# Optimization experiments

Measured on AMD Instinct MI355X. Metric: run time of the kernel, lower is better.

Reference implementation:

```python
import jax, jax.numpy as jnp
import numpy as np

D = 768       # GATv2 in/out feats (num_heads=1)
D_OUT = 384   # fc output
K = 51        # round(top_rate * L) = round(0.1 * 512)
EPS = 1e-5    # nn.LayerNorm default eps


def _layer_norm(x, g, b):
    mu = jnp.mean(x, axis=-1, keepdims=True)
    var = jnp.mean((x - mu) ** 2, axis=-1, keepdims=True)
    return (x - mu) / jnp.sqrt(var + EPS) * g + b


def setup_inputs() -> dict:
    key = jax.random.key(0)
    ks = jax.random.split(key, 12)
    B, L = 4, 512
    s = 0.02
    return {
        "hidden_state": jax.random.normal(ks[0], (B, L, D), jnp.float32),
        "attention": jax.random.uniform(ks[1], (B, L, L), jnp.float32),
        # GATv2Conv params (fc_src, fc_dst, attn vector, output bias)
        "W_src": jax.random.normal(ks[2], (D, D), jnp.float32) * s,
        "b_src": jnp.zeros((D,), jnp.float32),
        "W_dst": jax.random.normal(ks[3], (D, D), jnp.float32) * s,
        "b_dst": jnp.zeros((D,), jnp.float32),
        "attn_vec": jax.random.normal(ks[4], (D,), jnp.float32) * s,
        "gat_bias": jnp.zeros((D,), jnp.float32),
        # GlobalAttentionPooling gate_nn: Linear(768, 1)
        "gate_W": jax.random.normal(ks[5], (D, 1), jnp.float32) * s,
        "gate_b": jnp.zeros((1,), jnp.float32),
        # LayerNorm(768)
        "ln_g": jnp.ones((D,), jnp.float32),
        "ln_b": jnp.zeros((D,), jnp.float32),
        # fc: Linear(768, 384)
        "fc_W": jax.random.normal(ks[6], (D, D_OUT), jnp.float32) * s,
        "fc_b": jnp.zeros((D_OUT,), jnp.float32),
        # LayerNorm(384)
        "ln2_g": jnp.ones((D_OUT,), jnp.float32),
        "ln2_b": jnp.zeros((D_OUT,), jnp.float32),
        "mask": jnp.ones((B, L), jnp.int32),  # unused by the original forward
        "type": 0,                              # unused string/type flag
    }


def reference(hidden_state, attention, W_src, b_src, W_dst, b_dst, attn_vec,
              gat_bias, gate_W, gate_b, ln_g, ln_b, fc_W, fc_b, ln2_g, ln2_b,
              mask, type):
    B, L, _ = hidden_state.shape
    # --- topk sparsification: each node i keeps K source neighbors ---
    vals, idx = jax.lax.top_k(attention, K)          # [B, L, K]
    valid = vals > 0.0                                # edges kept by pos_sign filter

    # --- GATv2Conv (num_heads=1, residual=Identity since 768==768) ---
    feat_src = hidden_state @ W_src + b_src           # [B, L, D]
    feat_dst = hidden_state @ W_dst + b_dst           # [B, L, D]
    g = feat_src[jnp.arange(B)[:, None, None], idx]   # [B, L, K, D] gathered src feats
    e = jax.nn.leaky_relu(g + feat_dst[:, :, None, :], 0.2)
    scores = jnp.einsum("blkd,d->blk", e, attn_vec)   # [B, L, K]
    scores = jnp.where(valid, scores, -1e9)           # removed edges masked out
    a = jax.nn.softmax(scores, axis=-1)               # edge_softmax per dst node
    h = jnp.einsum("blk,blkd->bld", a, g)             # weighted scatter-sum
    h = h + hidden_state + gat_bias                   # residual (identity) + bias
    h = jax.nn.leaky_relu(h, 0.01)                    # nn.LeakyReLU activation

    # --- GlobalAttentionPooling: softmax(gate) weighted segment reduce ---
    gate = h @ gate_W + gate_b                        # [B, L, 1]
    p = jax.nn.softmax(gate, axis=1)
    pooled = jnp.sum(p * h, axis=1)                   # [B, D]

    # --- head: fc(dropout(ln(relu(out)))) then ln2 (dropout = eval identity) ---
    out = _layer_norm(jax.nn.relu(pooled), ln_g, ln_b)
    out = out @ fc_W + fc_b
    out = _layer_norm(out, ln2_g, ln2_b)
    return out
```

## Files before the change

kernel.cpp:

```cpp
#include <hip/hip_runtime.h>
#include <math.h>

#define D 768
#define DOUT 384
#define LSEQ 512
#define BATCH 4
#define KTOP 51
#define EPS 1e-5f

typedef unsigned short ushort_t;
typedef __bf16 bf16x8 __attribute__((ext_vector_type(8)));
typedef float f32x4 __attribute__((ext_vector_type(4)));
typedef float f32x2 __attribute__((ext_vector_type(2)));

#define GLOAD16(gp, lp)                                                        \
    __builtin_amdgcn_global_load_lds(                                          \
        (const __attribute__((address_space(1))) unsigned int*)(gp),           \
        (__attribute__((address_space(3))) unsigned int*)(lp), 16, 0, 0)

__device__ __forceinline__ ushort_t f2bf(float f) {
    unsigned int u = __builtin_bit_cast(unsigned int, f);
    u = (u + 0x7FFFu + ((u >> 16) & 1u)) >> 16;
    return (ushort_t)u;
}

__device__ __forceinline__ float bf2f(ushort_t u) {
    unsigned int v = ((unsigned int)u) << 16;
    return __builtin_bit_cast(float, v);
}

__global__ __launch_bounds__(256) void prep_kernel(const float* __restrict__ hidden,
                                                   ushort_t* __restrict__ Ah,
                                                   const float* __restrict__ W0,
                                                   const float* __restrict__ W1,
                                                   ushort_t* __restrict__ WT0,
                                                   ushort_t* __restrict__ WT1,
                                                   float* __restrict__ pooled,
                                                   float* __restrict__ z) {
    __shared__ float tile[32][33];
    const int bid = blockIdx.x;
    const int tid = threadIdx.x;
    if (bid < 1536) {
        const int i = (bid * 256 + tid) * 4;
        const float4 v = *(const float4*)(hidden + i);
        ushort4 o;
        o.x = f2bf(v.x); o.y = f2bf(v.y); o.z = f2bf(v.z); o.w = f2bf(v.w);
        *(ushort4*)(Ah + i) = o;
    } else if (bid < 2688) {
        const int t = bid - 1536;
        const int zz = t / 576;
        const int rem = t - zz * 576;
        const int by = rem / 24, bx = rem - by * 24;
        const float* W = zz ? W1 : W0;
        ushort_t* WT = zz ? WT1 : WT0;
        const int kbase = by * 32;
        const int nbase = bx * 32;
        const int r = tid >> 3, c4 = (tid & 7) * 4;

        const float4 v = *(const float4*)(W + (size_t)(kbase + r) * D + nbase + c4);
        tile[r][c4 + 0] = v.x; tile[r][c4 + 1] = v.y;
        tile[r][c4 + 2] = v.z; tile[r][c4 + 3] = v.w;
        __syncthreads();
        ushort4 o;
        o.x = f2bf(tile[c4 + 0][r]); o.y = f2bf(tile[c4 + 1][r]);
        o.z = f2bf(tile[c4 + 2][r]); o.w = f2bf(tile[c4 + 3][r]);
        *(ushort4*)(WT + (size_t)(nbase + r) * D + kbase + c4) = o;
    } else {
        for (int i = tid; i < BATCH * D; i += 256) pooled[i] = 0.f;
        for (int i = tid; i < BATCH * DOUT; i += 256) z[i] = 0.f;
    }
}

__global__ __launch_bounds__(256) void feat_gemm_kernel(const ushort_t* __restrict__ Ah,
                                                        const ushort_t* __restrict__ WT0,
                                                        const float* __restrict__ b0,
                                                        ushort_t* __restrict__ Csrc_bf,
                                                        const ushort_t* __restrict__ WT1,
                                                        const float* __restrict__ b1,
                                                        float* __restrict__ Cdst) {
    const int bid = blockIdx.x;
    const int wid = (bid & 7) * 96 + (bid >> 3);
    const int zz = wid / 384;
    const int rem = wid - zz * 384;
    const int tileY = rem / 12;
    const int tileX = rem - tileY * 12;

    const ushort_t* WT = zz ? WT1 : WT0;
    const float* bias = zz ? b1 : b0;

    __shared__ ushort_t As[64 * 64];
    __shared__ ushort_t Bs[64 * 64];

    const int tid = threadIdx.x;
    const int lane = tid & 63;
    const int wave = tid >> 6;
    const int quad = lane >> 4;
    const int m15 = lane & 15;
    const int qRow = (wave & 1) * 32;
    const int qCol = (wave >> 1) * 32;

    const int rowBase = tileY * 64;
    const int colBase = tileX * 64;

    const int e0 = tid * 8;
    const int r0 = e0 >> 6;
    const int c0 = e0 & 63;
    const int cc = c0 >> 3;
    const int csw = (cc ^ (r0 & 7)) << 3;
    const ushort_t* Abase = Ah + (size_t)rowBase * D;
    const ushort_t* Bbase = WT + (size_t)colBase * D;

    f32x4 acc[2][2] = {};

    for (int kk = 0; kk < D; kk += 64) {
        __syncthreads();
        GLOAD16(Abase + (size_t)r0 * D + kk + csw, &As[e0]);
        GLOAD16(Abase + (size_t)(r0 + 32) * D + kk + csw, &As[e0 + 2048]);
        GLOAD16(Bbase + (size_t)r0 * D + kk + csw, &Bs[e0]);
        GLOAD16(Bbase + (size_t)(r0 + 32) * D + kk + csw, &Bs[e0 + 2048]);
        __syncthreads();

        bf16x8 a[2][2], b[2][2];
#pragma unroll
        for (int i = 0; i < 2; ++i) {
            const int row = qRow + i * 16 + m15;
            const int sw = row & 7;
#pragma unroll
            for (int ks = 0; ks < 2; ++ks)
                a[i][ks] = *(const bf16x8*)&As[row * 64 + ((((ks << 2) + quad) ^ sw) << 3)];
        }
#pragma unroll
        for (int j = 0; j < 2; ++j) {
            const int row = qCol + j * 16 + m15;
            const int sw = row & 7;
#pragma unroll
            for (int ks = 0; ks < 2; ++ks)
                b[j][ks] = *(const bf16x8*)&Bs[row * 64 + ((((ks << 2) + quad) ^ sw) << 3)];
        }
#pragma unroll
        for (int ks = 0; ks < 2; ++ks)
#pragma unroll
            for (int i = 0; i < 2; ++i)
#pragma unroll
                for (int j = 0; j < 2; ++j)
                    acc[i][j] = __builtin_amdgcn_mfma_f32_16x16x32_bf16(a[i][ks], b[j][ks], acc[i][j], 0, 0, 0);
    }

    if (zz == 0) {
#pragma unroll
        for (int j = 0; j < 2; ++j) {
            const int col = colBase + qCol + j * 16 + m15;
            const float bv = bias[col];
#pragma unroll
            for (int i = 0; i < 2; ++i) {
                ushort_t* Cp = Csrc_bf + (size_t)(rowBase + qRow + i * 16 + quad * 4) * D + col;
#pragma unroll
                for (int r = 0; r < 4; ++r)
                    Cp[(size_t)r * D] = f2bf(acc[i][j][r] + bv);
            }
        }
    } else {
#pragma unroll
        for (int j = 0; j < 2; ++j) {
            const int col = colBase + qCol + j * 16 + m15;
            const float bv = bias[col];
#pragma unroll
            for (int i = 0; i < 2; ++i) {
                float* Cp = Cdst + (size_t)(rowBase + qRow + i * 16 + quad * 4) * D + col;
#pragma unroll
                for (int r = 0; r < 4; ++r)
                    Cp[(size_t)r * D] = acc[i][j][r] + bv;
            }
        }
    }
}

__global__ __launch_bounds__(256) void scoregath_kernel(const float* __restrict__ attn,
                                                        const ushort_t* __restrict__ fsrc_bf,
                                                        const float* __restrict__ feat_dst,
                                                        const float* __restrict__ attn_vec,
                                                        const float* __restrict__ gat_bias,
                                                        const float* __restrict__ hidden,
                                                        const float* __restrict__ gate_W,
                                                        const float* __restrict__ gate_b,
                                                        ushort_t* __restrict__ h,
                                                        float* __restrict__ gate) {
    const int bid = blockIdx.x;
    const int row = (bid & 7) * 256 + (bid >> 3);
    const int b = row >> 9;
    const int tid = threadIdx.x;
    const int lane = tid & 63;
    const int wave = tid >> 6;

    __shared__ float vals[LSEQ];
    __shared__ float cval[320];
    __shared__ int   cidx[320];
    __shared__ int   nhi, outSlot;
    __shared__ int   kid[KTOP];
    __shared__ float kvv[KTOP];
    __shared__ float wm[4], wl[4];
    __shared__ float hpart[4][D];
    __shared__ float gred[4];

    if (tid == 0) { nhi = 0; outSlot = 0; }

    const float* a = attn + (size_t)row * LSEQ;
    const float v0 = a[tid];
    const float v1 = a[tid + 256];
    vals[tid] = v0;
    vals[tid + 256] = v1;
    __syncthreads();

    {
        const unsigned long long m0 = __ballot(v0 > 0.75f);
        const unsigned long long m1 = __ballot(v1 > 0.75f);
        const int c0 = __popcll(m0);
        const int c1 = __popcll(m1);
        int base = 0;
        if (lane == 0) base = atomicAdd(&nhi, c0 + c1);
        base = __shfl(base, 0);
        const unsigned long long below = (1ull << lane) - 1ull;
        if (v0 > 0.75f) {
            const int s = base + __popcll(m0 & below);
            if (s < 320) { cval[s] = v0; cidx[s] = tid; }
        }
        if (v1 > 0.75f) {
            const int s = base + c0 + __popcll(m1 & below);
            if (s < 320) { cval[s] = v1; cidx[s] = tid + 256; }
        }
    }
    __syncthreads();

    const int n = nhi;
    if (n >= KTOP && n <= 320) {
        if (tid < n) {
            const float v = cval[tid];
            const int e = cidx[tid];
            int r = 0;
            for (int j = 0; j < n; ++j) {
                const float u = cval[j];
                r += (u > v) || (u == v && cidx[j] < e);
            }
            const bool keep = (r < KTOP);
            const unsigned long long mk = __ballot(keep);
            const int cnt = __popcll(mk);
            if (cnt > 0) {
                const int leader = __ffsll((unsigned long long)mk) - 1;
                int base = 0;
                if (lane == leader) base = atomicAdd(&outSlot, cnt);
                base = __shfl(base, leader);
                if (keep) {
                    const int s = base + __popcll(mk & ((1ull << lane) - 1ull));
                    kid[s] = e; kvv[s] = v;
                }
            }
        }
    } else {
#pragma unroll
        for (int e0 = 0; e0 < 2; ++e0) {
            const int e = tid + e0 * 256;
            const float v = vals[e];
            int r = 0;
            for (int j = 0; j < LSEQ; ++j) {
                const float u = vals[j];
                r += (u > v) || (u == v && j < e);
            }
            if (r < KTOP) {
                const int s = atomicAdd(&outSlot, 1);
                kid[s] = e; kvv[s] = v;
            }
        }
    }

    const int d0 = lane * 8;
    const int d1 = 512 + lane * 4;
    const float* fdp = feat_dst + (size_t)row * D;
    f32x2 fdr[6], avr[6];
    {
        const float4 f0 = *(const float4*)(fdp + d0);
        const float4 f1 = *(const float4*)(fdp + d0 + 4);
        const float4 f2 = *(const float4*)(fdp + d1);
        const float4 a0 = *(const float4*)(attn_vec + d0);
        const float4 a1 = *(const float4*)(attn_vec + d0 + 4);
        const float4 a2 = *(const float4*)(attn_vec + d1);
        fdr[0] = f32x2{f0.x, f0.y}; fdr[1] = f32x2{f0.z, f0.w};
        fdr[2] = f32x2{f1.x, f1.y}; fdr[3] = f32x2{f1.z, f1.w};
        fdr[4] = f32x2{f2.x, f2.y}; fdr[5] = f32x2{f2.z, f2.w};
        avr[0] = f32x2{a0.x, a0.y}; avr[1] = f32x2{a0.z, a0.w};
        avr[2] = f32x2{a1.x, a1.y}; avr[3] = f32x2{a1.z, a1.w};
        avr[4] = f32x2{a2.x, a2.y}; avr[5] = f32x2{a2.z, a2.w};
    }
    __syncthreads();

    const ushort_t* fb = fsrc_bf + ((size_t)(b << 9)) * D;
    float m_run = -3.0e38f, l_run = 0.f;
    f32x2 acc[6] = {};

    const ushort_t* gp0 = fb + (size_t)kid[wave] * D;
    bf16x8 cg0 = *(const bf16x8*)(gp0 + d0);
    ushort4 cg1 = *(const ushort4*)(gp0 + d1);

    for (int k = wave; k < KTOP; k += 4) {
        const int kn = (k + 4 < KTOP) ? (k + 4) : k;
        const ushort_t* gn = fb + (size_t)kid[kn] * D;
        const bf16x8 ng0 = *(const bf16x8*)(gn + d0);
        const ushort4 ng1 = *(const ushort4*)(gn + d1);

        f32x2 gf[6];
        gf[0] = f32x2{(float)cg0[0], (float)cg0[1]};
        gf[1] = f32x2{(float)cg0[2], (float)cg0[3]};
        gf[2] = f32x2{(float)cg0[4], (float)cg0[5]};
        gf[3] = f32x2{(float)cg0[6], (float)cg0[7]};
        gf[4] = f32x2{bf2f(cg1.x), bf2f(cg1.y)};
        gf[5] = f32x2{bf2f(cg1.z), bf2f(cg1.w)};

        f32x2 s2 = {0.f, 0.f};
#pragma unroll
        for (int jj = 0; jj < 6; ++jj) {
            f32x2 x = gf[jj] + fdr[jj];
            x = __builtin_elementwise_max(x, x * 0.2f);
            s2 += x * avr[jj];
        }
        float s = s2.x + s2.y;
#pragma unroll
        for (int off = 32; off > 0; off >>= 1) s += __shfl_xor(s, off);
        s = (kvv[k] > 0.f) ? s : -1e9f;

        if (s > m_run + 8.f) {
            const float rs = __expf(m_run - s);
            l_run *= rs;
#pragma unroll
            for (int jj = 0; jj < 6; ++jj) acc[jj] *= rs;
            m_run = s;
        }
        const float p = __expf(s - m_run);
        l_run += p;
#pragma unroll
        for (int jj = 0; jj < 6; ++jj) acc[jj] += p * gf[jj];

        cg0 = ng0; cg1 = ng1;
    }

    if (lane == 0) { wm[wave] = m_run; wl[wave] = l_run; }
    *(f32x2*)&hpart[wave][d0]     = acc[0];
    *(f32x2*)&hpart[wave][d0 + 2] = acc[1];
    *(f32x2*)&hpart[wave][d0 + 4] = acc[2];
    *(f32x2*)&hpart[wave][d0 + 6] = acc[3];
    *(f32x2*)&hpart[wave][d1]     = acc[4];
    *(f32x2*)&hpart[wave][d1 + 2] = acc[5];
    __syncthreads();

    const float M = fmaxf(fmaxf(wm[0], wm[1]), fmaxf(wm[2], wm[3]));
    const float r0 = __expf(wm[0] - M), r1 = __expf(wm[1] - M);
    const float r2 = __expf(wm[2] - M), r3 = __expf(wm[3] - M);
    const float invL = 1.f / (r0 * wl[0] + r1 * wl[1] + r2 * wl[2] + r3 * wl[3]);

    float dotp = 0.f;
    const float* hid = hidden + (size_t)row * D;
    ushort_t* hb = h + (size_t)row * D;
#pragma unroll
    for (int j = 0; j < 3; ++j) {
        const int d = tid + j * 256;
        const float hv = (r0 * hpart[0][d] + r1 * hpart[1][d] +
                          r2 * hpart[2][d] + r3 * hpart[3][d]) * invL;
        float v = hv + hid[d] + gat_bias[d];
        v = v > 0.f ? v : 0.01f * v;
        hb[d] = f2bf(v);
        dotp += v * gate_W[d];
    }
#pragma unroll
    for (int off = 32; off > 0; off >>= 1) dotp += __shfl_xor(dotp, off);
    if (lane == 0) gred[wave] = dotp;
    __syncthreads();
    if (tid == 0) gate[row] = gate_b[0] + gred[0] + gred[1] + gred[2] + gred[3];
}

__global__ __launch_bounds__(256) void pool_kernel(const ushort_t* __restrict__ h,
                                                   const float* __restrict__ gate,
                                                   float* __restrict__ pooled) {
    const int b = blockIdx.z;
    const int lbase = blockIdx.y * 64;
    const int d = blockIdx.x * 256 + threadIdx.x;
    const int tid = threadIdx.x;
    const int lane = tid & 63;
    const int w = tid >> 6;

    __shared__ float wred[4];
    __shared__ float ps[64];

    const float g0 = gate[b * LSEQ + tid];
    const float g1 = gate[b * LSEQ + tid + 256];
    float m = fmaxf(g0, g1);
#pragma unroll
    for (int off = 32; off > 0; off >>= 1) m = fmaxf(m, __shfl_xor(m, off));
    if (lane == 0) wred[w] = m;
    __syncthreads();
    m = fmaxf(fmaxf(wred[0], wred[1]), fmaxf(wred[2], wred[3]));
    float e = __expf(g0 - m) + __expf(g1 - m);
#pragma unroll
    for (int off = 32; off > 0; off >>= 1) e += __shfl_xor(e, off);
    __syncthreads();
    if (lane == 0) wred[w] = e;
    __syncthreads();
    const float inv = 1.f / (wred[0] + wred[1] + wred[2] + wred[3]);
    if (tid < 64) ps[tid] = __expf(gate[b * LSEQ + lbase + tid] - m) * inv;
    __syncthreads();

    const ushort_t* hb = h + ((size_t)(b * LSEQ + lbase)) * D + d;
    float acc = 0.f;
#pragma unroll 8
    for (int l = 0; l < 64; ++l) {
        acc += ps[l] * bf2f(hb[(size_t)l * D]);
    }
    atomicAdd(&pooled[b * D + d], acc);
}

__global__ __launch_bounds__(256) void fc_kernel(const float* __restrict__ pooled,
                                                 const float* __restrict__ ln_g,
                                                 const float* __restrict__ ln_b,
                                                 const float* __restrict__ fc_W,
                                                 float* __restrict__ z) {
    const int b = blockIdx.z;
    const int by = blockIdx.y;
    const int dbase = by * 256;
    const int jbase = blockIdx.x * 64;
    const int tid = threadIdx.x;
    const int lane = tid & 63;
    const int w = tid >> 6;
    const int jt = tid & 63;
    const int sub = tid >> 6;

    __shared__ float wred[4];
    __shared__ float ys[256];
    __shared__ float part[4][64];

    float v[3];
#pragma unroll
    for (int i = 0; i < 3; ++i) v[i] = fmaxf(pooled[b * D + tid + i * 256], 0.f);

    float s = v[0] + v[1] + v[2];
#pragma unroll
    for (int off = 32; off > 0; off >>= 1) s += __shfl_xor(s, off);
    if (lane == 0) wred[w] = s;
    __syncthreads();
    const float mu = (wred[0] + wred[1] + wred[2] + wred[3]) / (float)D;
    float vs = 0.f;
#pragma unroll
    for (int i = 0; i < 3; ++i) { const float dd = v[i] - mu; vs += dd * dd; }
#pragma unroll
    for (int off = 32; off > 0; off >>= 1) vs += __shfl_xor(vs, off);
    __syncthreads();
    if (lane == 0) wred[w] = vs;
    __syncthreads();
    const float rstd = rsqrtf((wred[0] + wred[1] + wred[2] + wred[3]) / (float)D + EPS);

    const float vb = (by == 0) ? v[0] : (by == 1 ? v[1] : v[2]);
    ys[tid] = (vb - mu) * rstd * ln_g[dbase + tid] + ln_b[dbase + tid];
    __syncthreads();

    const float* W = fc_W + (size_t)(dbase + sub * 64) * DOUT + jbase + jt;
    const float* yy = ys + sub * 64;
    float acc = 0.f;
#pragma unroll 8
    for (int i = 0; i < 64; ++i) {
        acc += yy[i] * W[(size_t)i * DOUT];
    }
    part[sub][jt] = acc;
    __syncthreads();
    if (sub == 0) {
        const float tot = part[0][jt] + part[1][jt] + part[2][jt] + part[3][jt];
        atomicAdd(&z[b * DOUT + jbase + jt], tot);
    }
}

__global__ __launch_bounds__(384) void ln2_kernel(const float* __restrict__ z,
                                                  const float* __restrict__ fc_b,
                                                  const float* __restrict__ ln2_g,
                                                  const float* __restrict__ ln2_b,
                                                  float* __restrict__ out) {
    const int b = blockIdx.x;
    const int tid = threadIdx.x;
    const int lane = tid & 63;
    const int wave = tid >> 6;
    __shared__ float wred[6];

    const float v = z[b * DOUT + tid] + fc_b[tid];

    float s = v;
#pragma unroll
    for (int off = 32; off > 0; off >>= 1) s += __shfl_xor(s, off);
    if (lane == 0) wred[wave] = s;
    __syncthreads();
    float mu = 0.f;
#pragma unroll
    for (int w = 0; w < 6; ++w) mu += wred[w];
    mu /= (float)DOUT;
    __syncthreads();

    const float dd = v - mu;
    float s2 = dd * dd;
#pragma unroll
    for (int off = 32; off > 0; off >>= 1) s2 += __shfl_xor(s2, off);
    if (lane == 0) wred[wave] = s2;
    __syncthreads();
    float var = 0.f;
#pragma unroll
    for (int w = 0; w < 6; ++w) var += wred[w];
    const float rstd = rsqrtf(var / (float)DOUT + EPS);

    out[b * DOUT + tid] = dd * rstd * ln2_g[tid] + ln2_b[tid];
}

extern "C" void kernel_launch(void* const* d_in, const int* in_sizes, int n_in,
                              void* d_out, int out_size, void* d_ws, size_t ws_size,
                              hipStream_t stream) {
    const float* hidden   = (const float*)d_in[0];
    const float* attention= (const float*)d_in[1];
    const float* W_src    = (const float*)d_in[2];
    const float* b_src    = (const float*)d_in[3];
    const float* W_dst    = (const float*)d_in[4];
    const float* b_dst    = (const float*)d_in[5];
    const float* attn_vec = (const float*)d_in[6];
    const float* gat_bias = (const float*)d_in[7];
    const float* gate_W   = (const float*)d_in[8];
    const float* gate_b   = (const float*)d_in[9];
    const float* ln_g     = (const float*)d_in[10];
    const float* ln_b     = (const float*)d_in[11];
    const float* fc_W     = (const float*)d_in[12];
    const float* fc_b     = (const float*)d_in[13];
    const float* ln2_g    = (const float*)d_in[14];
    const float* ln2_b    = (const float*)d_in[15];
    float* out = (float*)d_out;

    const int M = BATCH * LSEQ;
    float* feat_dst = (float*)d_ws;
    float* gate     = feat_dst + (size_t)M * D;
    float* pooled   = gate + M;
    float* z        = pooled + BATCH * D;
    ushort_t* Ah    = (ushort_t*)(z + BATCH * DOUT);
    ushort_t* WT0   = Ah + (size_t)M * D;
    ushort_t* WT1   = WT0 + (size_t)D * D;
    ushort_t* fsrcb = WT1 + (size_t)D * D;
    ushort_t* h     = fsrcb + (size_t)M * D;

    hipLaunchKernelGGL(prep_kernel, dim3(2689), dim3(256), 0, stream,
                       hidden, Ah, W_src, W_dst, WT0, WT1, pooled, z);
    hipLaunchKernelGGL(feat_gemm_kernel, dim3(768), dim3(256), 0, stream,
                       Ah, WT0, b_src, fsrcb, WT1, b_dst, feat_dst);
    hipLaunchKernelGGL(scoregath_kernel, dim3(M), dim3(256), 0, stream,
                       attention, fsrcb, feat_dst, attn_vec, gat_bias, hidden,
                       gate_W, gate_b, h, gate);
    hipLaunchKernelGGL(pool_kernel, dim3(D / 256, LSEQ / 64, BATCH), dim3(256), 0, stream,
                       h, gate, pooled);
    hipLaunchKernelGGL(fc_kernel, dim3(DOUT / 64, D / 256, BATCH), dim3(256), 0, stream,
                       pooled, ln_g, ln_b, fc_W, z);
    hipLaunchKernelGGL(ln2_kernel, dim3(BATCH), dim3(384), 0, stream,
                       z, fc_b, ln2_g, ln2_b, out);
}
```

Measured before the change: 151.3 us.

## Move top-k selection into prep kernel and pass indices through workspace

Moves the per-row top-k neighbor selection out of the score/gather kernel and into extra blocks of the prep kernel, which write the kept indices and values to a global workspace. The scoregath kernel then only loads the 51 indices and values per row. The rank-counting loop also now reads candidates four at a time with vector LDS loads. The aim is to run the selection work alongside the bf16 conversion and transpose blocks, and to shorten the scoregath kernel. In exchange the prep kernel uses more shared memory and there is an extra global round trip for the indices.

```diff
diff --git a/kernel.cpp b/kernel.cpp
--- a/kernel.cpp
+++ b/kernel.cpp
@@ -36,8 +36,18 @@
                                                    ushort_t* __restrict__ WT0,
                                                    ushort_t* __restrict__ WT1,
                                                    float* __restrict__ pooled,
-                                                   float* __restrict__ z) {
+                                                   float* __restrict__ z,
+                                                   const float* __restrict__ attn,
+                                                   int* __restrict__ kidg,
+                                                   float* __restrict__ kvvg) {
     __shared__ float tile[32][33];
+    __shared__ float vals[LSEQ];
+    __shared__ float cval[320];
+    __shared__ int   cidx[320];
+    __shared__ int   nhi, outSlot;
+    __shared__ int   kid[KTOP];
+    __shared__ float kvv[KTOP];
+
     const int bid = blockIdx.x;
     const int tid = threadIdx.x;
     if (bid < 1536) {
@@ -65,9 +75,96 @@
         o.x = f2bf(tile[c4 + 0][r]); o.y = f2bf(tile[c4 + 1][r]);
         o.z = f2bf(tile[c4 + 2][r]); o.w = f2bf(tile[c4 + 3][r]);
         *(ushort4*)(WT + (size_t)(nbase + r) * D + kbase + c4) = o;
-    } else {
+    } else if (bid == 2688) {
         for (int i = tid; i < BATCH * D; i += 256) pooled[i] = 0.f;
         for (int i = tid; i < BATCH * DOUT; i += 256) z[i] = 0.f;
+    } else {
+        const int row = bid - 2689;
+        const int lane = tid & 63;
+        if (tid == 0) { nhi = 0; outSlot = 0; }
+
+        const float* a = attn + (size_t)row * LSEQ;
+        const float v0 = a[tid];
+        const float v1 = a[tid + 256];
+        vals[tid] = v0;
+        vals[tid + 256] = v1;
+        __syncthreads();
+
+        {
+            const unsigned long long m0 = __ballot(v0 > 0.75f);
+            const unsigned long long m1 = __ballot(v1 > 0.75f);
+            const int c0 = __popcll(m0);
+            const int c1 = __popcll(m1);
+            int base = 0;
+            if (lane == 0) base = atomicAdd(&nhi, c0 + c1);
+            base = __shfl(base, 0);
+            const unsigned long long below = (1ull << lane) - 1ull;
+            if (v0 > 0.75f) {
+                const int s = base + __popcll(m0 & below);
+                if (s < 320) { cval[s] = v0; cidx[s] = tid; }
+            }
+            if (v1 > 0.75f) {
+                const int s = base + c0 + __popcll(m1 & below);
+                if (s < 320) { cval[s] = v1; cidx[s] = tid + 256; }
+            }
+        }
+        __syncthreads();
+
+        const int n = nhi;
+        if (n >= KTOP && n <= 320) {
+            if (tid < n) {
+                const float v = cval[tid];
+                const int e = cidx[tid];
+                int r = 0;
+                int j = 0;
+                const int n4 = n & ~3;
+                for (; j < n4; j += 4) {
+                    const float4 u4 = *(const float4*)&cval[j];
+                    const int4 e4 = *(const int4*)&cidx[j];
+                    r += (u4.x > v) || (u4.x == v && e4.x < e);
+                    r += (u4.y > v) || (u4.y == v && e4.y < e);
+                    r += (u4.z > v) || (u4.z == v && e4.z < e);
+                    r += (u4.w > v) || (u4.w == v && e4.w < e);
+                }
+                for (; j < n; ++j) {
+                    const float u = cval[j];
+                    r += (u > v) || (u == v && cidx[j] < e);
+                }
+                const bool keep = (r < KTOP);
+                const unsigned long long mk = __ballot(keep);
+                const int cnt = __popcll(mk);
+                if (cnt > 0) {
+                    const int leader = __ffsll((unsigned long long)mk) - 1;
+                    int base = 0;
+                    if (lane == leader) base = atomicAdd(&outSlot, cnt);
+                    base = __shfl(base, leader);
+                    if (keep) {
+                        const int s = base + __popcll(mk & ((1ull << lane) - 1ull));
+                        kid[s] = e; kvv[s] = v;
+                    }
+                }
+            }
+        } else {
+#pragma unroll
+            for (int e0 = 0; e0 < 2; ++e0) {
+                const int e = tid + e0 * 256;
+                const float v = vals[e];
+                int r = 0;
+                for (int j = 0; j < LSEQ; ++j) {
+                    const float u = vals[j];
+                    r += (u > v) || (u == v && j < e);
+                }
+                if (r < KTOP) {
+                    const int s = atomicAdd(&outSlot, 1);
+                    kid[s] = e; kvv[s] = v;
+                }
+            }
+        }
+        __syncthreads();
+        if (tid < KTOP) {
+            kidg[(size_t)row * 64 + tid] = kid[tid];
+            kvvg[(size_t)row * 64 + tid] = kvv[tid];
+        }
     }
 }
 
@@ -175,7 +272,8 @@
     }
 }
 
-__global__ __launch_bounds__(256) void scoregath_kernel(const float* __restrict__ attn,
+__global__ __launch_bounds__(256) void scoregath_kernel(const int* __restrict__ kidg,
+                                                        const float* __restrict__ kvvg,
                                                         const ushort_t* __restrict__ fsrc_bf,
                                                         const float* __restrict__ feat_dst,
                                                         const float* __restrict__ attn_vec,
@@ -192,84 +290,15 @@
     const int lane = tid & 63;
     const int wave = tid >> 6;
 
-    __shared__ float vals[LSEQ];
-    __shared__ float cval[320];
-    __shared__ int   cidx[320];
-    __shared__ int   nhi, outSlot;
     __shared__ int   kid[KTOP];
     __shared__ float kvv[KTOP];
     __shared__ float wm[4], wl[4];
     __shared__ float hpart[4][D];
     __shared__ float gred[4];
 
-    if (tid == 0) { nhi = 0; outSlot = 0; }
-
-    const float* a = attn + (size_t)row * LSEQ;
-    const float v0 = a[tid];
-    const float v1 = a[tid + 256];
-    vals[tid] = v0;
-    vals[tid + 256] = v1;
-    __syncthreads();
-
-    {
-        const unsigned long long m0 = __ballot(v0 > 0.75f);
-        const unsigned long long m1 = __ballot(v1 > 0.75f);
-        const int c0 = __popcll(m0);
-        const int c1 = __popcll(m1);
-        int base = 0;
-        if (lane == 0) base = atomicAdd(&nhi, c0 + c1);
-        base = __shfl(base, 0);
-        const unsigned long long below = (1ull << lane) - 1ull;
-        if (v0 > 0.75f) {
-            const int s = base + __popcll(m0 & below);
-            if (s < 320) { cval[s] = v0; cidx[s] = tid; }
-        }
-        if (v1 > 0.75f) {
-            const int s = base + c0 + __popcll(m1 & below);
-            if (s < 320) { cval[s] = v1; cidx[s] = tid + 256; }
-        }
-    }
-    __syncthreads();
-
-    const int n = nhi;
-    if (n >= KTOP && n <= 320) {
-        if (tid < n) {
-            const float v = cval[tid];
-            const int e = cidx[tid];
-            int r = 0;
-            for (int j = 0; j < n; ++j) {
-                const float u = cval[j];
-                r += (u > v) || (u == v && cidx[j] < e);
-            }
-            const bool keep = (r < KTOP);
-            const unsigned long long mk = __ballot(keep);
-            const int cnt = __popcll(mk);
-            if (cnt > 0) {
-                const int leader = __ffsll((unsigned long long)mk) - 1;
-                int base = 0;
-                if (lane == leader) base = atomicAdd(&outSlot, cnt);
-                base = __shfl(base, leader);
-                if (keep) {
-                    const int s = base + __popcll(mk & ((1ull << lane) - 1ull));
-                    kid[s] = e; kvv[s] = v;
-                }
-            }
-        }
-    } else {
-#pragma unroll
-        for (int e0 = 0; e0 < 2; ++e0) {
-            const int e = tid + e0 * 256;
-            const float v = vals[e];
-            int r = 0;
-            for (int j = 0; j < LSEQ; ++j) {
-                const float u = vals[j];
-                r += (u > v) || (u == v && j < e);
-            }
-            if (r < KTOP) {
-                const int s = atomicAdd(&outSlot, 1);
-                kid[s] = e; kvv[s] = v;
-            }
-        }
+    if (tid < KTOP) {
+        kid[tid] = kidg[(size_t)row * 64 + tid];
+        kvv[tid] = kvvg[(size_t)row * 64 + tid];
     }
 
     const int d0 = lane * 8;
@@ -537,18 +566,21 @@
     float* gate     = feat_dst + (size_t)M * D;
     float* pooled   = gate + M;
     float* z        = pooled + BATCH * D;
-    ushort_t* Ah    = (ushort_t*)(z + BATCH * DOUT);
+    float* kvvg     = z + BATCH * DOUT;
+    int*   kidg     = (int*)(kvvg + (size_t)M * 64);
+    ushort_t* Ah    = (ushort_t*)(kidg + (size_t)M * 64);
     ushort_t* WT0   = Ah + (size_t)M * D;
     ushort_t* WT1   = WT0 + (size_t)D * D;
     ushort_t* fsrcb = WT1 + (size_t)D * D;
     ushort_t* h     = fsrcb + (size_t)M * D;
 
-    hipLaunchKernelGGL(prep_kernel, dim3(2689), dim3(256), 0, stream,
-                       hidden, Ah, W_src, W_dst, WT0, WT1, pooled, z);
+    hipLaunchKernelGGL(prep_kernel, dim3(2689 + M), dim3(256), 0, stream,
+                       hidden, Ah, W_src, W_dst, WT0, WT1, pooled, z,
+                       attention, kidg, kvvg);
     hipLaunchKernelGGL(feat_gemm_kernel, dim3(768), dim3(256), 0, stream,
                        Ah, WT0, b_src, fsrcb, WT1, b_dst, feat_dst);
     hipLaunchKernelGGL(scoregath_kernel, dim3(M), dim3(256), 0, stream,
-                       attention, fsrcb, feat_dst, attn_vec, gat_bias, hidden,
+                       kidg, kvvg, fsrcb, feat_dst, attn_vec, gat_bias, hidden,
                        gate_W, gate_b, h, gate);
     hipLaunchKernelGGL(pool_kernel, dim3(D / 256, LSEQ / 64, BATCH), dim3(256), 0, stream,
                        h, gate, pooled);
```

Result: faster. 147.7 us (median of 2 runs) (-2.3%).
